# Performance work log

Measured on AMD Instinct MI355X. Metric: run time of the kernel, lower is better.

Reference implementation:

```python
import jax, jax.numpy as jnp
import numpy as np

B, S, D, H, HD = 4, 2048, 1024, 16, 64  # batch, seq, d_model, heads, head_dim


def setup_inputs() -> dict:
    key = jax.random.key(0)
    ks = jax.random.split(key, 9)
    scale = 0.02
    x = jax.random.normal(ks[0], (B, S, D), jnp.float32)
    Wq = jax.random.normal(ks[1], (D, H, HD), jnp.float32) * scale
    Wk = jax.random.normal(ks[2], (D, H, HD), jnp.float32) * scale
    Wv = jax.random.normal(ks[3], (D, H, HD), jnp.float32) * scale
    bq = jax.random.normal(ks[4], (H, HD), jnp.float32) * scale
    bk = jax.random.normal(ks[5], (H, HD), jnp.float32) * scale
    bv = jax.random.normal(ks[6], (H, HD), jnp.float32) * scale
    Wo = jax.random.normal(ks[7], (H, HD, D), jnp.float32) * scale
    bo = jax.random.normal(ks[8], (D,), jnp.float32) * scale
    return {"x": x, "Wq": Wq, "bq": bq, "Wk": Wk, "bk": bk,
            "Wv": Wv, "bv": bv, "Wo": Wo, "bo": bo}


def reference(x, Wq, bq, Wk, bk, Wv, bv, Wo, bo):
    # QKV projections -> (B, S, H, HD)
    q = jnp.einsum("bsd,dhe->bshe", x, Wq) + bq
    k = jnp.einsum("bsd,dhe->bshe", x, Wk) + bk
    v = jnp.einsum("bsd,dhe->bshe", x, Wv) + bv
    # scaled dot-product attention (deterministic, no mask/bias)
    q = q / jnp.sqrt(jnp.asarray(HD, q.dtype))
    scores = jnp.einsum("bqhd,bkhd->bhqk", q, k)  # (B, H, S, S)
    attn = jax.nn.softmax(scores, axis=-1)
    ctx = jnp.einsum("bhqk,bkhd->bqhd", attn, v)  # (B, S, H, HD)
    # output projection -> (B, S, D)
    return jnp.einsum("bqhd,hdo->bqo", ctx, Wo) + bo
```

## Files before the change

kernel.cpp:

```cpp
#include <hip/hip_runtime.h>


typedef unsigned short u16;
typedef __attribute__((ext_vector_type(4))) float f32x4;
typedef __attribute__((ext_vector_type(8))) short s16x8;
typedef __attribute__((ext_vector_type(4))) unsigned short u16x4;
typedef __attribute__((ext_vector_type(2))) unsigned int u32x2;
typedef __attribute__((ext_vector_type(4))) unsigned int u32x4;

#define DEV __device__ __forceinline__

#if __has_builtin(__builtin_amdgcn_exp2f)
#define EXP2(x) __builtin_amdgcn_exp2f(x)
#else
#define EXP2(x) exp2f(x)
#endif

DEV u16 f2b(float f) {
  unsigned u = __float_as_uint(f);
  u += 0x7fffu + ((u >> 16) & 1u);
  return (u16)(u >> 16);
}

DEV unsigned pack2(float a, float b) {
#if __has_builtin(__builtin_amdgcn_cvt_pk_bf16_f32)
  typedef __attribute__((ext_vector_type(2))) __bf16 bf16x2;
  bf16x2 r = __builtin_amdgcn_cvt_pk_bf16_f32(a, b);
  return __builtin_bit_cast(unsigned, r);
#else
  return (unsigned)f2b(a) | ((unsigned)f2b(b) << 16);
#endif
}

DEV void async16(const void* g, void* l) {
  __builtin_amdgcn_global_load_lds(
      (const __attribute__((address_space(1))) unsigned int*)g,
      (__attribute__((address_space(3))) unsigned int*)l, 16, 0, 0);
}

__global__ void k_cast(const float* __restrict__ x, u16* __restrict__ xb) {
  int i = (blockIdx.x * 256 + threadIdx.x) * 4;
  float4 v = *(const float4*)(x + i);
  u16x4 o;
  o.x = f2b(v.x); o.y = f2b(v.y); o.z = f2b(v.z); o.w = f2b(v.w);
  *(u16x4*)(xb + i) = o;
}

__global__ void k_packw_all(const float* __restrict__ Wq, const float* __restrict__ Wk,
                            const float* __restrict__ Wv, const float* __restrict__ Wo,
                            u16* __restrict__ wt, u16* __restrict__ wot, float qscale) {
  const float* src; u16* dst; float scale = 1.0f;
  switch (blockIdx.z) {
    case 0: src = Wq; dst = wt; scale = qscale; break;
    case 1: src = Wk; dst = wt + 1024 * 1024; break;
    case 2: src = Wv; dst = wt + 2 * 1024 * 1024; break;
    default: src = Wo; dst = wot; break;
  }
  __shared__ float tile[32][33];
  int t = threadIdx.x;
  int k0 = blockIdx.x * 32, n0 = blockIdx.y * 32;
  int c = t & 31, r0 = t >> 5;
#pragma unroll
  for (int p = 0; p < 4; ++p) {
    int r = p * 8 + r0;
    tile[r][c] = src[(size_t)(k0 + r) * 1024 + n0 + c] * scale;
  }
  __syncthreads();
#pragma unroll
  for (int p = 0; p < 4; ++p) {
    int r = p * 8 + r0;
    dst[(size_t)(n0 + r) * 1024 + k0 + c] = f2b(tile[c][r]);
  }
}

__global__ void k_packbias(const float* __restrict__ bq, const float* __restrict__ bk,
                           const float* __restrict__ bv, float* __restrict__ out,
                           float qscale) {
  int t = blockIdx.x * 256 + threadIdx.x;
  float v = (t < 1024) ? bq[t] * qscale : (t < 2048 ? bk[t - 1024] : bv[t - 2048]);
  out[t] = v;
}

template <int MODE>
__global__ __launch_bounds__(256, 2) void k_gemm_bt(
    const u16* __restrict__ A, const u16* __restrict__ Bt,
    const float* __restrict__ bias, void* __restrict__ Cout, u16* __restrict__ VT,
    int K, int ldC, int nbase) {
  __shared__ u16 SH[16384];
  u16* As = SH;
  u16* Bs = SH + 8192;
  const int t = threadIdx.x;
  const int w = t >> 6, l = t & 63;
  const int lane15 = l & 15, quad = l >> 4;
  const int m0 = blockIdx.x * 128, n0 = nbase + blockIdx.y * 128;
  const int wm = (w >> 1) * 64, wn = (w & 1) * 64;

  const int srow = t >> 3, cp = t & 7;
  const u16* aSrc[4]; const u16* bSrc[4]; int ldsOff[4];
#pragma unroll
  for (int i = 0; i < 4; ++i) {
    int row = i * 32 + srow;
    int gc = cp ^ (row & 7);
    aSrc[i] = A + (size_t)(m0 + row) * K + gc * 8;
    bSrc[i] = Bt + (size_t)(n0 + row) * K + gc * 8;
    ldsOff[i] = (i * 32 + w * 8) * 64;
  }

  f32x4 acc[4][4] = {};

  for (int kk = 0; kk < K; kk += 64) {
#pragma unroll
    for (int i = 0; i < 4; ++i) async16(aSrc[i] + kk, As + ldsOff[i]);
#pragma unroll
    for (int i = 0; i < 4; ++i) async16(bSrc[i] + kk, Bs + ldsOff[i]);
    __builtin_amdgcn_s_waitcnt(0);
    __syncthreads();

#pragma unroll
    for (int ks = 0; ks < 2; ++ks) {
      s16x8 af[4], bf[4];
#pragma unroll
      for (int mi = 0; mi < 4; ++mi) {
        int r = wm + mi * 16 + lane15;
        int c = ks * 4 + quad;
        af[mi] = *(const s16x8*)(As + r * 64 + (c ^ (r & 7)) * 8);
      }
#pragma unroll
      for (int ni = 0; ni < 4; ++ni) {
        int r = wn + ni * 16 + lane15;
        int c = ks * 4 + quad;
        bf[ni] = *(const s16x8*)(Bs + r * 64 + (c ^ (r & 7)) * 8);
      }
#pragma unroll
      for (int mi = 0; mi < 4; ++mi)
#pragma unroll
        for (int ni = 0; ni < 4; ++ni)
          acc[mi][ni] = (MODE == 0)
              ? __builtin_amdgcn_mfma_f32_16x16x32_bf16(bf[ni], af[mi], acc[mi][ni], 0, 0, 0)
              : __builtin_amdgcn_mfma_f32_16x16x32_bf16(af[mi], bf[ni], acc[mi][ni], 0, 0, 0);
    }
    __syncthreads();
  }

  if (MODE == 0) {
    u16* W = SH + w * 4096;
#pragma unroll
    for (int ni = 0; ni < 4; ++ni) {
      int gnb = n0 + wn + ni * 16 + quad * 4;
      float4 bb = *(const float4*)(bias + gnb);
#pragma unroll
      for (int mi = 0; mi < 4; ++mi) {
        int mloc = mi * 16 + lane15;
        int nloc = ni * 16 + quad * 4;
        int blk = (nloc >> 3) ^ (mloc & 7);
        u32x2 o;
        o.x = pack2(acc[mi][ni][0] + bb.x, acc[mi][ni][1] + bb.y);
        o.y = pack2(acc[mi][ni][2] + bb.z, acc[mi][ni][3] + bb.w);
        *(u32x2*)(W + mloc * 64 + blk * 8 + (quad & 1) * 4) = o;
      }
    }
    const int l8 = l & 7, lr = l >> 3;
#pragma unroll
    for (int it = 0; it < 8; ++it) {
      int mloc = it * 8 + lr;
      int lb = l8 ^ (mloc & 7);
      s16x8 v = *(const s16x8*)(W + mloc * 64 + l8 * 8);
      int gm = m0 + wm + mloc;
      *(s16x8*)((u16*)Cout + (size_t)gm * ldC + n0 + wn + lb * 8) = v;
    }
  } else if (MODE == 1) {
#pragma unroll
    for (int ni = 0; ni < 4; ++ni) {
      int gn = n0 + wn + ni * 16 + lane15;
      float bb = bias[gn];
#pragma unroll
      for (int mi = 0; mi < 4; ++mi) {
        int gmBase = m0 + wm + mi * 16 + quad * 4;
#pragma unroll
        for (int r = 0; r < 4; ++r)
          ((float*)Cout)[(size_t)(gmBase + r) * ldC + gn] = acc[mi][ni][r] + bb;
      }
    }
  } else {
    u16* W = SH + w * 4096;
#pragma unroll
    for (int ni = 0; ni < 4; ++ni) {
      int gn = n0 + wn + ni * 16 + lane15;
      float bb = bias[gn];
#pragma unroll
      for (int mi = 0; mi < 4; ++mi) {
        int nloc = ni * 16 + lane15;
        int mloc = mi * 16 + quad * 4;
        int blk = (mloc >> 3) ^ (nloc & 7);
        u32x2 o;
        o.x = pack2(acc[mi][ni][0] + bb, acc[mi][ni][1] + bb);
        o.y = pack2(acc[mi][ni][2] + bb, acc[mi][ni][3] + bb);
        *(u32x2*)(W + nloc * 64 + blk * 8 + (quad & 1) * 4) = o;
      }
    }
    const int l8 = l & 7, lr = l >> 3;
#pragma unroll
    for (int it = 0; it < 8; ++it) {
      int nloc = it * 8 + lr;
      int lb = l8 ^ (nloc & 7);
      s16x8 v = *(const s16x8*)(W + nloc * 64 + l8 * 8);
      int gv = (n0 - 2048) + wn + nloc;
      int hh = gv >> 6, hd = gv & 63;
      int gm = m0 + wm + lb * 8;
      int bb2 = gm >> 11, s = gm & 2047;
      *(s16x8*)(VT + (((size_t)(bb2 * 16 + hh) * 64 + hd) * 2048 + s)) = v;
    }
  }
}

__global__ __launch_bounds__(256, 2) void k_flash(
    const u16* __restrict__ qkv, const u16* __restrict__ vt, u16* __restrict__ ctx) {
  __shared__ u16 S[2][8192];
  const int t = threadIdx.x;
  const int w = t >> 6, l = t & 63;
  const int lane15 = l & 15, quad = l >> 4;
  const int bh = blockIdx.x, qt = blockIdx.y;
  const int b = bh >> 4, h = bh & 15;

  int qrow[4];
  s16x8 qf[4][2];
#pragma unroll
  for (int T = 0; T < 4; ++T) {
    qrow[T] = b * 2048 + qt * 256 + T * 64 + w * 16 + lane15;
    const u16* qp = qkv + (size_t)qrow[T] * 2048 + h * 64 + quad * 8;
    qf[T][0] = *(const s16x8*)(qp);
    qf[T][1] = *(const s16x8*)(qp + 32);
  }

  const int srow = t >> 3, cp = t & 7;
  const u16* kSrc[2]; const u16* vSrc[2]; int kOff[2]; int vOff[2];
#pragma unroll
  for (int i = 0; i < 2; ++i) {
    int row = i * 32 + srow;
    int xk = (row & 3) | (((row >> 3) & 1) << 2);
    kSrc[i] = qkv + (size_t)(b * 2048 + row) * 2048 + 1024 + h * 64 + (cp ^ xk) * 8;
    vSrc[i] = vt + (size_t)bh * (64 * 2048) + (size_t)row * 2048 + (cp ^ (row & 7)) * 8;
    kOff[i] = (i * 32 + w * 8) * 64;
    vOff[i] = 4096 + (i * 32 + w * 8) * 64;
  }

  const int kr = (lane15 >> 2) * 8 + (lane15 & 3);
  f32x4 O[4][4] = {};
  f32x4 sacc[4] = {};
  const f32x4 ZERO4 = {};
  const u32x4 onesu = {0x3F803F80u, 0x3F803F80u, 0x3F803F80u, 0x3F803F80u};
  const s16x8 onesf = __builtin_bit_cast(s16x8, onesu);

#pragma unroll
  for (int i = 0; i < 2; ++i) async16(kSrc[i], &S[0][kOff[i]]);
#pragma unroll
  for (int i = 0; i < 2; ++i) async16(vSrc[i], &S[0][vOff[i]]);

  for (int jt = 0; jt < 32; ++jt) {
    __builtin_amdgcn_s_waitcnt(0);
    __syncthreads();
    const u16* Sb = S[jt & 1];
    if (jt < 31) {
      const size_t kAdv = (size_t)(jt + 1) * 64 * 2048;
      const int vAdv = (jt + 1) * 64;
      u16* D = S[(jt & 1) ^ 1];
#pragma unroll
      for (int i = 0; i < 2; ++i) async16(kSrc[i] + kAdv, D + kOff[i]);
#pragma unroll
      for (int i = 0; i < 2; ++i) async16(vSrc[i] + vAdv, D + vOff[i]);
    }

    f32x4 st[4][4];
#pragma unroll
    for (int tt = 0; tt < 4; ++tt) {
      int rr = kr + (tt & 1) * 4 + (tt >> 1) * 32;
      int xk = (rr & 3) | (((rr >> 3) & 1) << 2);
      s16x8 kf = *(const s16x8*)(Sb + rr * 64 + ((0 * 4 + quad) ^ xk) * 8);
#pragma unroll
      for (int T = 0; T < 4; ++T)
        st[T][tt] = __builtin_amdgcn_mfma_f32_16x16x32_bf16(kf, qf[T][0], ZERO4, 0, 0, 0);
    }
#pragma unroll
    for (int tt = 0; tt < 4; ++tt) {
      int rr = kr + (tt & 1) * 4 + (tt >> 1) * 32;
      int xk = (rr & 3) | (((rr >> 3) & 1) << 2);
      s16x8 kf = *(const s16x8*)(Sb + rr * 64 + ((1 * 4 + quad) ^ xk) * 8);
#pragma unroll
      for (int T = 0; T < 4; ++T)
        st[T][tt] = __builtin_amdgcn_mfma_f32_16x16x32_bf16(kf, qf[T][1], st[T][tt], 0, 0, 0);
    }

#pragma unroll
    for (int ks = 0; ks < 2; ++ks) {
      s16x8 pf[4];
#pragma unroll
      for (int T = 0; T < 4; ++T) {
        float p0 = EXP2(st[T][2 * ks][0]), p1 = EXP2(st[T][2 * ks][1]);
        float p2 = EXP2(st[T][2 * ks][2]), p3 = EXP2(st[T][2 * ks][3]);
        float p4 = EXP2(st[T][2 * ks + 1][0]), p5 = EXP2(st[T][2 * ks + 1][1]);
        float p6 = EXP2(st[T][2 * ks + 1][2]), p7 = EXP2(st[T][2 * ks + 1][3]);
        u32x4 pu = {pack2(p0, p1), pack2(p2, p3), pack2(p4, p5), pack2(p6, p7)};
        pf[T] = __builtin_bit_cast(s16x8, pu);
        sacc[T] = __builtin_amdgcn_mfma_f32_16x16x32_bf16(onesf, pf[T], sacc[T], 0, 0, 0);
      }
      const u16* Vh = Sb + 4096;
      int c7 = ks * 4 + quad;
#pragma unroll
      for (int co = 0; co < 4; ++co) {
        int rr = co * 16 + lane15;
        s16x8 vf = *(const s16x8*)(Vh + rr * 64 + ((c7 ^ (rr & 7))) * 8);
#pragma unroll
        for (int T = 0; T < 4; ++T)
          O[T][co] = __builtin_amdgcn_mfma_f32_16x16x32_bf16(vf, pf[T], O[T][co], 0, 0, 0);
      }
    }
  }

#pragma unroll
  for (int T = 0; T < 4; ++T) {
    float inv = 1.0f / sacc[T][0];
#pragma unroll
    for (int co = 0; co < 4; ++co) {
      u32x2 o;
      o.x = pack2(O[T][co][0] * inv, O[T][co][1] * inv);
      o.y = pack2(O[T][co][2] * inv, O[T][co][3] * inv);
      *(u32x2*)(ctx + (size_t)qrow[T] * 1024 + h * 64 + co * 16 + quad * 4) = o;
    }
  }
}

static constexpr size_t OFF_XB  = 0;
static constexpr size_t OFF_WT  = OFF_XB + (16u << 20);
static constexpr size_t OFF_WOT = OFF_WT + (6u << 20);
static constexpr size_t OFF_B3  = OFF_WOT + (2u << 20);
static constexpr size_t OFF_QKV = OFF_B3 + (1u << 20);
static constexpr size_t OFF_VT  = OFF_QKV + (32u << 20);
static constexpr size_t OFF_CTX = OFF_VT + (16u << 20);

extern "C" void kernel_launch(void* const* d_in, const int* in_sizes, int n_in,
                              void* d_out, int out_size, void* d_ws, size_t ws_size,
                              hipStream_t stream) {
  const float* x  = (const float*)d_in[0];
  const float* Wq = (const float*)d_in[1];
  const float* bq = (const float*)d_in[2];
  const float* Wk = (const float*)d_in[3];
  const float* bk = (const float*)d_in[4];
  const float* Wv = (const float*)d_in[5];
  const float* bv = (const float*)d_in[6];
  const float* Wo = (const float*)d_in[7];
  const float* bo = (const float*)d_in[8];
  char* ws = (char*)d_ws;
  u16* xb    = (u16*)(ws + OFF_XB);
  u16* wt    = (u16*)(ws + OFF_WT);
  u16* wot   = (u16*)(ws + OFF_WOT);
  float* b3  = (float*)(ws + OFF_B3);
  u16* qkv   = (u16*)(ws + OFF_QKV);
  u16* vtb   = (u16*)(ws + OFF_VT);
  u16* ctx   = (u16*)(ws + OFF_CTX);
  float* out = (float*)d_out;

  const float QSCALE = 0.125f * 1.44269504f;

  k_cast<<<8192, 256, 0, stream>>>(x, xb);
  k_packw_all<<<dim3(32, 32, 4), 256, 0, stream>>>(Wq, Wk, Wv, Wo, wt, wot, QSCALE);
  k_packbias<<<12, 256, 0, stream>>>(bq, bk, bv, b3, QSCALE);
  k_gemm_bt<0><<<dim3(64, 16), 256, 0, stream>>>(xb, wt, b3, qkv, nullptr, 1024, 2048, 0);
  k_gemm_bt<2><<<dim3(64, 8), 256, 0, stream>>>(xb, wt, b3, nullptr, vtb, 1024, 2048, 2048);
  k_flash<<<dim3(64, 8), 256, 0, stream>>>(qkv, vtb, ctx);
  k_gemm_bt<1><<<dim3(64, 8), 256, 0, stream>>>(ctx, wot, bo, out, nullptr, 1024, 1024, 0);
}
```

Measured before the change: 261.6 us.

## Double-buffer GEMM LDS tiles, compute softmax row sums in VALU, add MFMA priority hints

The projection GEMM now keeps two LDS tile buffers and prefetches the next K-slice while computing on the current one, so global loads overlap with MFMA work. The attention kernel drops the extra ones-vector MFMA used for the softmax denominator. Instead it accumulates the sums in scalar registers from the fp32 exponentials and reduces them across lanes with shuffles at the end. It also raises wave priority around the MFMA blocks via s_setprio. LDS use per GEMM block doubles, which may reduce occupancy. The denominator now comes from unrounded fp32 values, not bf16-rounded ones.

```diff
diff --git a/kernel.cpp b/kernel.cpp
--- a/kernel.cpp
+++ b/kernel.cpp
@@ -86,9 +86,7 @@
     const u16* __restrict__ A, const u16* __restrict__ Bt,
     const float* __restrict__ bias, void* __restrict__ Cout, u16* __restrict__ VT,
     int K, int ldC, int nbase) {
-  __shared__ u16 SH[16384];
-  u16* As = SH;
-  u16* Bs = SH + 8192;
+  __shared__ u16 SH[32768];
   const int t = threadIdx.x;
   const int w = t >> 6, l = t & 63;
   const int lane15 = l & 15, quad = l >> 4;
@@ -107,14 +105,27 @@
   }
 
   f32x4 acc[4][4] = {};
-
-  for (int kk = 0; kk < K; kk += 64) {
-#pragma unroll
-    for (int i = 0; i < 4; ++i) async16(aSrc[i] + kk, As + ldsOff[i]);
-#pragma unroll
-    for (int i = 0; i < 4; ++i) async16(bSrc[i] + kk, Bs + ldsOff[i]);
-    __builtin_amdgcn_s_waitcnt(0);
-    __syncthreads();
+  const int nIter = K >> 6;
+
+#pragma unroll
+  for (int i = 0; i < 4; ++i) async16(aSrc[i], SH + ldsOff[i]);
+#pragma unroll
+  for (int i = 0; i < 4; ++i) async16(bSrc[i], SH + 8192 + ldsOff[i]);
+  __builtin_amdgcn_s_waitcnt(0);
+  __syncthreads();
+
+  int cur = 0;
+  for (int it = 0; it < nIter; ++it) {
+    const u16* As = SH + cur * 16384;
+    const u16* Bs = As + 8192;
+    if (it + 1 < nIter) {
+      const int kk = (it + 1) * 64;
+      u16* Ad = SH + (cur ^ 1) * 16384;
+#pragma unroll
+      for (int i = 0; i < 4; ++i) async16(aSrc[i] + kk, Ad + ldsOff[i]);
+#pragma unroll
+      for (int i = 0; i < 4; ++i) async16(bSrc[i] + kk, Ad + 8192 + ldsOff[i]);
+    }
 
 #pragma unroll
     for (int ks = 0; ks < 2; ++ks) {
@@ -139,7 +150,10 @@
               ? __builtin_amdgcn_mfma_f32_16x16x32_bf16(bf[ni], af[mi], acc[mi][ni], 0, 0, 0)
               : __builtin_amdgcn_mfma_f32_16x16x32_bf16(af[mi], bf[ni], acc[mi][ni], 0, 0, 0);
     }
+
+    if (it + 1 < nIter) __builtin_amdgcn_s_waitcnt(0);
     __syncthreads();
+    cur ^= 1;
   }
 
   if (MODE == 0) {
@@ -246,10 +260,8 @@
 
   const int kr = (lane15 >> 2) * 8 + (lane15 & 3);
   f32x4 O[4][4] = {};
-  f32x4 sacc[4] = {};
+  float lsum[4] = {0.0f, 0.0f, 0.0f, 0.0f};
   const f32x4 ZERO4 = {};
-  const u32x4 onesu = {0x3F803F80u, 0x3F803F80u, 0x3F803F80u, 0x3F803F80u};
-  const s16x8 onesf = __builtin_bit_cast(s16x8, onesu);
 
 #pragma unroll
   for (int i = 0; i < 2; ++i) async16(kSrc[i], &S[0][kOff[i]]);
@@ -271,6 +283,7 @@
     }
 
     f32x4 st[4][4];
+    __builtin_amdgcn_s_setprio(1);
 #pragma unroll
     for (int tt = 0; tt < 4; ++tt) {
       int rr = kr + (tt & 1) * 4 + (tt >> 1) * 32;
@@ -289,6 +302,7 @@
       for (int T = 0; T < 4; ++T)
         st[T][tt] = __builtin_amdgcn_mfma_f32_16x16x32_bf16(kf, qf[T][1], st[T][tt], 0, 0, 0);
     }
+    __builtin_amdgcn_s_setprio(0);
 
 #pragma unroll
     for (int ks = 0; ks < 2; ++ks) {
@@ -299,12 +313,13 @@
         float p2 = EXP2(st[T][2 * ks][2]), p3 = EXP2(st[T][2 * ks][3]);
         float p4 = EXP2(st[T][2 * ks + 1][0]), p5 = EXP2(st[T][2 * ks + 1][1]);
         float p6 = EXP2(st[T][2 * ks + 1][2]), p7 = EXP2(st[T][2 * ks + 1][3]);
+        lsum[T] += ((p0 + p1) + (p2 + p3)) + ((p4 + p5) + (p6 + p7));
         u32x4 pu = {pack2(p0, p1), pack2(p2, p3), pack2(p4, p5), pack2(p6, p7)};
         pf[T] = __builtin_bit_cast(s16x8, pu);
-        sacc[T] = __builtin_amdgcn_mfma_f32_16x16x32_bf16(onesf, pf[T], sacc[T], 0, 0, 0);
       }
       const u16* Vh = Sb + 4096;
       int c7 = ks * 4 + quad;
+      __builtin_amdgcn_s_setprio(1);
 #pragma unroll
       for (int co = 0; co < 4; ++co) {
         int rr = co * 16 + lane15;
@@ -313,12 +328,19 @@
         for (int T = 0; T < 4; ++T)
           O[T][co] = __builtin_amdgcn_mfma_f32_16x16x32_bf16(vf, pf[T], O[T][co], 0, 0, 0);
       }
+      __builtin_amdgcn_s_setprio(0);
     }
   }
 
 #pragma unroll
   for (int T = 0; T < 4; ++T) {
-    float inv = 1.0f / sacc[T][0];
+    lsum[T] += __shfl_xor(lsum[T], 16);
+    lsum[T] += __shfl_xor(lsum[T], 32);
+  }
+
+#pragma unroll
+  for (int T = 0; T < 4; ++T) {
+    float inv = 1.0f / lsum[T];
 #pragma unroll
     for (int co = 0; co < 4; ++co) {
       u32x2 o;
```

Result: slower. 266.9 us (+2.0%).
